# Optimization experiments

Hardware: AMD Instinct MI355X
Metric: run time of the kernel (lower is better)

## Reference

```python
import jax, jax.numpy as jnp
import numpy as np

B, Q, DIM, HEADS, RPE_H, HGRID, WGRID, STRIDE = 2, 900, 256, 8, 512, 64, 64, 16
KV = HGRID * WGRID


def setup_inputs() -> dict:
    key = jax.random.key(0)
    ks = jax.random.split(key, 16)
    s = 0.02
    return {
        "hidden_states": jax.random.normal(ks[0], (B, Q, DIM), jnp.float32),
        "reference_points": jax.random.uniform(ks[1], (B, Q, 1, 4), jnp.float32),
        "key_value_states": jax.random.normal(ks[2], (B, KV, DIM), jnp.float32),
        "spatial_shapes": jnp.array([[HGRID, WGRID]], dtype=jnp.int64),
        "attention_mask": jax.random.randint(ks[3], (B, KV), 0, 2, jnp.int32),
        "mlp1_w1": jax.random.normal(ks[4], (RPE_H, 2), jnp.float32) * s,
        "mlp1_b1": jnp.zeros((RPE_H,), jnp.float32),
        "mlp1_w2": jax.random.normal(ks[5], (HEADS, RPE_H), jnp.float32) * s,
        "mlp2_w1": jax.random.normal(ks[6], (RPE_H, 2), jnp.float32) * s,
        "mlp2_b1": jnp.zeros((RPE_H,), jnp.float32),
        "mlp2_w2": jax.random.normal(ks[7], (HEADS, RPE_H), jnp.float32) * s,
        "q_w": jax.random.normal(ks[8], (DIM, DIM), jnp.float32) * s,
        "q_b": jnp.zeros((DIM,), jnp.float32),
        "k_w": jax.random.normal(ks[9], (DIM, DIM), jnp.float32) * s,
        "k_b": jnp.zeros((DIM,), jnp.float32),
        "v_w": jax.random.normal(ks[10], (DIM, DIM), jnp.float32) * s,
        "v_b": jnp.zeros((DIM,), jnp.float32),
        "o_w": jax.random.normal(ks[11], (DIM, DIM), jnp.float32) * s,
        "o_b": jnp.zeros((DIM,), jnp.float32),
    }


def _attn(hidden_states, reference_points, key_value_states, h, w, attention_mask,
          mlp1_w1, mlp1_b1, mlp1_w2, mlp2_w1, mlp2_b1, mlp2_w2,
          q_w, q_b, k_w, k_b, v_w, v_b, o_w, o_b):
    b, q_len, dim = hidden_states.shape
    nh = mlp1_w2.shape[0]
    hd = dim // nh
    scale = hd ** -0.5
    stride = STRIDE

    # boxes cxcywh -> x1y1x2y2, scaled to absolute pixel coords (reparam=False)
    c, sz = reference_points[..., :2], reference_points[..., 2:]
    ref = jnp.concatenate([c - sz / 2, c + sz / 2], axis=-1)  # (B,Q,1,4)
    mult = jnp.array([w * stride, h * stride, w * stride, h * stride], dtype=ref.dtype)
    ref = ref * mult

    pos_x = (jnp.arange(w, dtype=jnp.float32) + 0.5) * stride
    pos_y = (jnp.arange(h, dtype=jnp.float32) + 0.5) * stride
    dx = ref[..., 0::2] - pos_x[None, None, :, None]  # (B,Q,W,2)
    dy = ref[..., 1::2] - pos_y[None, None, :, None]  # (B,Q,H,2)

    # small MLPs: 2 -> rpe_hidden -> num_heads
    rpe_x = jax.nn.relu(dx @ mlp1_w1.T + mlp1_b1) @ mlp1_w2.T  # (B,Q,W,nh)
    rpe_y = jax.nn.relu(dy @ mlp2_w1.T + mlp2_b1) @ mlp2_w2.T  # (B,Q,H,nh)
    rpe = rpe_x[:, :, None, :, :] + rpe_y[:, :, :, None, :]    # (B,Q,H,W,nh)
    rpe = rpe.reshape(b, q_len, h * w, nh).transpose(0, 3, 1, 2)  # (B,nh,Q,K)

    queries = (hidden_states @ q_w.T + q_b).reshape(b, q_len, nh, hd).transpose(0, 2, 1, 3) * scale
    kv_len = key_value_states.shape[1]
    keys = (key_value_states @ k_w.T + k_b).reshape(b, kv_len, nh, hd).transpose(0, 2, 1, 3)
    values = (key_value_states @ v_w.T + v_b).reshape(b, kv_len, nh, hd).transpose(0, 2, 1, 3)

    scores = jnp.einsum('bhqd,bhkd->bhqk', queries, keys) + rpe
    scores = scores + attention_mask.astype(scores.dtype)[:, None, None] * (-100.0)
    probs = jax.nn.softmax(scores, axis=-1)
    ctx = jnp.einsum('bhqk,bhkd->bhqd', probs, values)
    ctx = ctx.transpose(0, 2, 1, 3).reshape(b, q_len, dim)
    return ctx @ o_w.T + o_b


def reference(hidden_states, reference_points, key_value_states, spatial_shapes, attention_mask,
              mlp1_w1, mlp1_b1, mlp1_w2, mlp2_w1, mlp2_b1, mlp2_w2,
              q_w, q_b, k_w, k_b, v_w, v_b, o_w, o_b):
    h = int(spatial_shapes[0, 0])
    w = int(spatial_shapes[0, 1])
    return _attn(hidden_states, reference_points, key_value_states, h, w, attention_mask,
                 mlp1_w1, mlp1_b1, mlp1_w2, mlp2_w1, mlp2_b1, mlp2_w2,
                 q_w, q_b, k_w, k_b, v_w, v_b, o_w, o_b)
```

## Files before the change

### kernel.cpp

```cpp
#include <hip/hip_runtime.h>
#include <math.h>

#define NB    2
#define NQ    900
#define NQP   960
#define NKV   4096
#define DIMM  256
#define NHEAD 8
#define HD    32
#define RPEH  512
#define GRID  64

#define LOG2E 1.4426950408889634f

typedef short short8 __attribute__((ext_vector_type(8)));
typedef float f32x4 __attribute__((ext_vector_type(4)));
typedef unsigned uint2v __attribute__((ext_vector_type(2)));
typedef unsigned short u16;
typedef unsigned short u16x4 __attribute__((ext_vector_type(4)));

__device__ inline u16 f2bf(float f) {
    unsigned u = __builtin_bit_cast(unsigned, f);
    u += 0x7fff + ((u >> 16) & 1);
    return (u16)(u >> 16);
}
__device__ inline unsigned packbf2(float a, float b) {
    unsigned ua = __builtin_bit_cast(unsigned, a);
    ua += 0x7fff + ((ua >> 16) & 1);
    unsigned ub = __builtin_bit_cast(unsigned, b);
    ub += 0x7fff + ((ub >> 16) & 1);
    return (ua >> 16) | (ub & 0xffff0000u);
}

#define HS4  115200
#define KV4  524288
#define W4   16384
__global__ __launch_bounds__(256) void conv_bf16(
    const float* __restrict__ hs, const float* __restrict__ kv,
    const float* __restrict__ qw, const float* __restrict__ kw,
    const float* __restrict__ vw,
    u16* __restrict__ hsbf, u16* __restrict__ kvbf,
    u16* __restrict__ qwbf, u16* __restrict__ kwbf, u16* __restrict__ vwbf)
{
    const int total = HS4 + KV4 + 3 * W4;
    for (int g = blockIdx.x * 256 + threadIdx.x; g < total; g += gridDim.x * 256) {
        const float* s; u16* d; int off;
        if (g < HS4)                       { s = hs; d = hsbf; off = g; }
        else if (g < HS4 + KV4)            { s = kv; d = kvbf; off = g - HS4; }
        else if (g < HS4 + KV4 + W4)       { s = qw; d = qwbf; off = g - HS4 - KV4; }
        else if (g < HS4 + KV4 + 2 * W4)   { s = kw; d = kwbf; off = g - HS4 - KV4 - W4; }
        else                               { s = vw; d = vwbf; off = g - HS4 - KV4 - 2 * W4; }
        f32x4 v = *(const f32x4*)(s + (size_t)off * 4);
        *(u16x4*)(d + (size_t)off * 4) =
            (u16x4){f2bf(v[0]), f2bf(v[1]), f2bf(v[2]), f2bf(v[3])};
    }
}

__global__ __launch_bounds__(256) void proj_mfma(
    const u16* __restrict__ A,
    const u16* __restrict__ W0, const float* __restrict__ B0,
    const u16* __restrict__ W1, const float* __restrict__ B1,
    u16* __restrict__ outRow, u16* __restrict__ outVt,
    int M, float scale)
{
    __shared__ u16 Abuf[2][4096];
    __shared__ u16 Bbuf[2][4096];

    const u16* W = W0; const float* bias = B0; bool vt = false;
    if (blockIdx.z == 1) { W = W1; bias = B1; vt = true; }

    const int t    = threadIdx.x;
    const int lane = t & 63;
    const int w    = t >> 6;
    const int wm   = w >> 1, wn = w & 1;
    const int m0   = blockIdx.x * 128;
    const int n0   = blockIdx.y * 128;

    const int r0 = t >> 2, c0 = t & 3;
    const int r1 = r0 + 64;
    const int s0 = r0 * 4 + (c0 ^ (r0 & 3));
    const int s1 = r1 * 4 + (c0 ^ (r1 & 3));
    const u16* Arow0 = A + (size_t)(m0 + r0) * DIMM + c0 * 8;
    const u16* Arow1 = A + (size_t)(m0 + r1) * DIMM + c0 * 8;
    const u16* Wrow0 = W + (size_t)(n0 + r0) * DIMM + c0 * 8;
    const u16* Wrow1 = W + (size_t)(n0 + r1) * DIMM + c0 * 8;

    const int fr = lane & 15, fkc = lane >> 4;
    int aslot[4], bslot[4];
    #pragma unroll
    for (int f = 0; f < 4; ++f) {
        int ar = wm * 64 + f * 16 + fr;
        int br = wn * 64 + f * 16 + fr;
        aslot[f] = ar * 4 + (fkc ^ (ar & 3));
        bslot[f] = br * 4 + (fkc ^ (br & 3));
    }
    float bv[4];
    #pragma unroll
    for (int f = 0; f < 4; ++f) bv[f] = bias[n0 + wn * 64 + f * 16 + fr];

    f32x4 acc[4][4] = {};

    {
        short8 a0 = *(const short8*)(Arow0);
        short8 a1 = *(const short8*)(Arow1);
        short8 b0 = *(const short8*)(Wrow0);
        short8 b1 = *(const short8*)(Wrow1);
        *(short8*)&Abuf[0][s0 * 8] = a0;
        *(short8*)&Abuf[0][s1 * 8] = a1;
        *(short8*)&Bbuf[0][s0 * 8] = b0;
        *(short8*)&Bbuf[0][s1 * 8] = b1;
    }
    __syncthreads();

    int cur = 0;
    for (int kt = 0; kt < 8; ++kt) {
        short8 na0, na1, nb0, nb1;
        if (kt < 7) {
            int ko = (kt + 1) * 32;
            na0 = *(const short8*)(Arow0 + ko);
            na1 = *(const short8*)(Arow1 + ko);
            nb0 = *(const short8*)(Wrow0 + ko);
            nb1 = *(const short8*)(Wrow1 + ko);
        }
        short8 af[4], bf[4];
        #pragma unroll
        for (int f = 0; f < 4; ++f) {
            af[f] = *(const short8*)&Abuf[cur][aslot[f] * 8];
            bf[f] = *(const short8*)&Bbuf[cur][bslot[f] * 8];
        }
        #pragma unroll
        for (int i = 0; i < 4; ++i)
            #pragma unroll
            for (int j = 0; j < 4; ++j)
                acc[i][j] = __builtin_amdgcn_mfma_f32_16x16x32_bf16(af[i], bf[j], acc[i][j], 0, 0, 0);
        if (kt < 7) {
            *(short8*)&Abuf[cur ^ 1][s0 * 8] = na0;
            *(short8*)&Abuf[cur ^ 1][s1 * 8] = na1;
            *(short8*)&Bbuf[cur ^ 1][s0 * 8] = nb0;
            *(short8*)&Bbuf[cur ^ 1][s1 * 8] = nb1;
        }
        __syncthreads();
        cur ^= 1;
    }

    #pragma unroll
    for (int i = 0; i < 4; ++i) {
        int mbase = m0 + wm * 64 + i * 16 + 4 * fkc;
        #pragma unroll
        for (int j = 0; j < 4; ++j) {
            int n = n0 + wn * 64 + j * 16 + fr;
            #pragma unroll
            for (int r = 0; r < 4; ++r) {
                int gm = mbase + r;
                if (gm < M) {
                    float v = (acc[i][j][r] + bv[j]) * scale;
                    if (!vt) {
                        outRow[(size_t)gm * DIMM + n] = f2bf(v);
                    } else {
                        int bb = gm >> 12, kvi = gm & 4095;
                        int hh = n >> 5, dd = n & 31;
                        outVt[(size_t)((bb * NHEAD + hh) * HD + dd) * NKV + kvi] = f2bf(v);
                    }
                }
            }
        }
    }
}

__global__ __launch_bounds__(256) void rpe_kernel(
    const float* __restrict__ ref_pts,
    const float* __restrict__ w1x, const float* __restrict__ b1x,
    const float* __restrict__ w2x,
    const float* __restrict__ w1y, const float* __restrict__ b1y,
    const float* __restrict__ w2y,
    float* __restrict__ rpex, float* __restrict__ rpey)
{
    __shared__ f32x4 wpk[RPEH];
    __shared__ float w2t[RPEH][NHEAD];
    __shared__ float2 red[3][4][4][64];

    const int t   = threadIdx.x;
    const int m   = blockIdx.x & 1;
    const int bq0 = (blockIdx.x >> 1) * 4;

    const float* w1 = m ? w1y : w1x;
    const float* b1 = m ? b1y : b1x;
    const float* w2 = m ? w2y : w2x;
    for (int r = t; r < RPEH; r += 256) {
        float a = w1[r * 2], b = w1[r * 2 + 1];
        wpk[r] = (f32x4){a, b, b1[r], a + b};
    }
    for (int i = t; i < RPEH * NHEAD; i += 256) {
        int h = i >> 9, r = i & 511;
        w2t[r][h] = w2[h * RPEH + r] * LOG2E;
    }
    __syncthreads();

    const int lane = t & 63;
    const int wv   = t >> 6;
    const float p  = (lane + 0.5f) * 16.f;

    float lo[4], hi[4];
    #pragma unroll
    for (int j = 0; j < 4; ++j) {
        const float* q = ref_pts + (size_t)(bq0 + j) * 4;
        float c = m ? q[1] : q[0];
        float s = m ? q[3] : q[2];
        lo[j] = (c - s * 0.5f) * 1024.f;
        hi[j] = (c + s * 0.5f) * 1024.f;
    }

    float2 acc[4][4] = {};
    const int r0 = wv * 128;
    #pragma unroll 4
    for (int rr = 0; rr < 128; ++rr) {
        int r = r0 + rr;
        f32x4 W  = wpk[r];
        f32x4 u0 = *(const f32x4*)&w2t[r][0];
        f32x4 u1 = *(const f32x4*)&w2t[r][4];
        float bp = W[3] * p;
        #pragma unroll
        for (int tk = 0; tk < 4; ++tk) {
            float al  = W[0] * lo[tk] + W[1] * hi[tk] + W[2];
            float hid = fmaxf(al - bp, 0.f);
            acc[tk][0].x += u0[0] * hid;  acc[tk][0].y += u0[1] * hid;
            acc[tk][1].x += u0[2] * hid;  acc[tk][1].y += u0[3] * hid;
            acc[tk][2].x += u1[0] * hid;  acc[tk][2].y += u1[1] * hid;
            acc[tk][3].x += u1[2] * hid;  acc[tk][3].y += u1[3] * hid;
        }
    }

    if (wv > 0) {
        #pragma unroll
        for (int tk = 0; tk < 4; ++tk)
            #pragma unroll
            for (int j = 0; j < 4; ++j)
                red[wv - 1][tk][j][lane] = acc[tk][j];
    }
    __syncthreads();
    if (wv == 0) {
        float* outp = m ? rpey : rpex;
        #pragma unroll
        for (int tk = 0; tk < 4; ++tk) {
            size_t base = (size_t)(bq0 + tk) * (NHEAD * GRID) + lane;
            #pragma unroll
            for (int j = 0; j < 4; ++j) {
                float2 s0 = red[0][tk][j][lane];
                float2 s1 = red[1][tk][j][lane];
                float2 s2 = red[2][tk][j][lane];
                float sx = acc[tk][j].x + s0.x + s1.x + s2.x;
                float sy = acc[tk][j].y + s0.y + s1.y + s2.y;
                outp[base + (2 * j) * GRID]     = sx;
                outp[base + (2 * j + 1) * GRID] = sy;
            }
        }
    }
}

template <int SPL>
__global__ __launch_bounds__(256) void attn_mfma(
    const u16* __restrict__ Qbf, const u16* __restrict__ Kbf,
    const u16* __restrict__ Vt,
    const float* __restrict__ RX, const float* __restrict__ RY,
    const int* __restrict__ mask,
    float* __restrict__ pctx, float2* __restrict__ pml)
{
    constexpr int KSEG = NKV / SPL;
    constexpr int NTS  = KSEG / 64;
    __shared__ short8 kbuf[2][4][64];
    __shared__ short8 vbuf[2][4][64];
    __shared__ unsigned pbuf[4][64][4];
    __shared__ float ry_s[NTS][68];
    __shared__ float mbuf[2][64];

    const int tid  = threadIdx.x;
    const int lane = tid & 63;
    const int w    = tid >> 6;
    const int q15  = lane & 15;
    const int g    = lane >> 4;
    const int qt = blockIdx.x, h = blockIdx.y;
    const int b  = blockIdx.z / SPL;
    const int sp = blockIdx.z % SPL;
    const int q0 = qt * 64;
    const int wq = w * 16 + q15;
    const int gq = q0 + wq;
    const bool qok = gq < NQ;
    const int kv0g = sp * KSEG;

    float rxr[16];
    {
        const float* rxrow = RX + (size_t)(b * NQ + (qok ? gq : 0)) * (NHEAD * GRID) + h * GRID;
        #pragma unroll
        for (int kt = 0; kt < 4; ++kt)
            #pragma unroll
            for (int r = 0; r < 4; ++r)
                rxr[kt * 4 + r] = qok ? rxrow[16 * kt + 4 * g + r] : 0.f;
    }
    for (int idx = tid; idx < NTS * 64; idx += 256) {
        int y = idx % NTS, q = idx / NTS;
        int gq2 = q0 + q;
        ry_s[y][q] = (gq2 < NQ)
            ? RY[(size_t)(b * NQ + gq2) * (NHEAD * GRID) + h * GRID + sp * NTS + y] : 0.f;
    }

    short8 qf = *(const short8*)(Qbf + ((size_t)(b * NQ + gq)) * DIMM + h * HD + 8 * g);

    const int sr = tid >> 2, sc = tid & 3;
    const int vd = tid >> 3, vc = tid & 7;
    const size_t kbase = ((size_t)(b * NKV + kv0g + sr)) * DIMM + h * HD + 8 * sc;
    const size_t vbase = ((size_t)((b * NHEAD + h) * HD + vd)) * NKV + kv0g + 8 * vc;

    kbuf[0][sr >> 4][(sr & 15) + 16 * sc] = *(const short8*)(Kbf + kbase);
    vbuf[0][(vc >> 2) * 2 + (vd >> 4)][16 * (vc & 3) + (vd & 15)] = *(const short8*)(Vt + vbase);
    if (tid < 64) mbuf[0][tid] = -(100.f * LOG2E) * (float)mask[b * NKV + kv0g + tid];
    __syncthreads();

    f32x4 cacc0 = {0.f, 0.f, 0.f, 0.f};
    f32x4 cacc1 = {0.f, 0.f, 0.f, 0.f};
    float m_run = -1e30f, l_run = 0.f;
    int cur = 0;

    for (int t = 0; t < NTS; ++t) {
        short8 rk = {}, rv = {};
        float rm = 0.f;
        if (t < NTS - 1) {
            size_t kvn = (size_t)(t + 1) * 64;
            rk = *(const short8*)(Kbf + kbase + kvn * DIMM);
            rv = *(const short8*)(Vt + vbase + kvn);
            if (tid < 64) rm = -(100.f * LOG2E) * (float)mask[b * NKV + kv0g + kvn + tid];
        }

        f32x4 zero = {0.f, 0.f, 0.f, 0.f};
        f32x4 s[4];
        __builtin_amdgcn_s_setprio(1);
        #pragma unroll
        for (int kt = 0; kt < 4; ++kt)
            s[kt] = __builtin_amdgcn_mfma_f32_16x16x32_bf16(kbuf[cur][kt][lane], qf, zero, 0, 0, 0);
        __builtin_amdgcn_s_setprio(0);

        float ryb = ry_s[t][wq];
        #pragma unroll
        for (int kt = 0; kt < 4; ++kt) {
            #pragma unroll
            for (int r = 0; r < 4; ++r)
                s[kt][r] += rxr[kt * 4 + r] + ryb + mbuf[cur][16 * kt + 4 * g + r];
        }

        float mk[4];
        #pragma unroll
        for (int kt = 0; kt < 4; ++kt)
            mk[kt] = fmaxf(fmaxf(s[kt][0], s[kt][1]), fmaxf(s[kt][2], s[kt][3]));
        float mloc = fmaxf(fmaxf(mk[0], mk[1]), fmaxf(mk[2], mk[3]));
        mloc = fmaxf(mloc, __shfl_xor(mloc, 16));
        mloc = fmaxf(mloc, __shfl_xor(mloc, 32));
        float mnew = fmaxf(m_run, mloc);
        float fsc  = exp2f(m_run - mnew);
        float psum = 0.f;
        #pragma unroll
        for (int kt = 0; kt < 4; ++kt)
            #pragma unroll
            for (int r = 0; r < 4; ++r) {
                float pv = exp2f(s[kt][r] - mnew);
                s[kt][r] = pv;
                psum += pv;
            }
        psum += __shfl_xor(psum, 16);
        psum += __shfl_xor(psum, 32);
        l_run = l_run * fsc + psum;
        m_run = mnew;
        cacc0 *= fsc;
        cacc1 *= fsc;

        __builtin_amdgcn_s_setprio(1);
        #pragma unroll
        for (int sk = 0; sk < 2; ++sk) {
            #pragma unroll
            for (int kk = 0; kk < 2; ++kk) {
                int kt = sk * 2 + kk;
                unsigned d0 = packbf2(s[kt][0], s[kt][1]);
                unsigned d1 = packbf2(s[kt][2], s[kt][3]);
                int lt = 16 * ((2 * kt + (g >> 1)) & 3) + q15;
                uint2v* dst = (uint2v*)&pbuf[w][lt][2 * (g & 1)];
                *dst = (uint2v){d0, d1};
            }
            short8 pf = *(const short8*)&pbuf[w][lane][0];
            cacc0 = __builtin_amdgcn_mfma_f32_16x16x32_bf16(vbuf[cur][sk * 2 + 0][lane], pf, cacc0, 0, 0, 0);
            cacc1 = __builtin_amdgcn_mfma_f32_16x16x32_bf16(vbuf[cur][sk * 2 + 1][lane], pf, cacc1, 0, 0, 0);
        }
        __builtin_amdgcn_s_setprio(0);

        if (t < NTS - 1) {
            kbuf[cur ^ 1][sr >> 4][(sr & 15) + 16 * sc] = rk;
            vbuf[cur ^ 1][(vc >> 2) * 2 + (vd >> 4)][16 * (vc & 3) + (vd & 15)] = rv;
            if (tid < 64) mbuf[cur ^ 1][tid] = rm;
        }
        __syncthreads();
        cur ^= 1;
    }

    size_t prow = (size_t)(sp * NB + b) * NQP + gq;
    float* pc = pctx + prow * DIMM + h * HD;
    #pragma unroll
    for (int r = 0; r < 4; ++r) {
        pc[4 * g + r]      = cacc0[r];
        pc[16 + 4 * g + r] = cacc1[r];
    }
    if (g == 0) {
        float2 v; v.x = m_run; v.y = l_run;
        pml[prow * NHEAD + h] = v;
    }
}

template <int SPL>
__global__ __launch_bounds__(256) void attn_reduce(
    const float* __restrict__ pctx, const float2* __restrict__ pml,
    float* __restrict__ CTX)
{
    const int bq = blockIdx.x;
    const int b = bq / NQ, q = bq - b * NQ;
    const int c = threadIdx.x;
    const int h = c >> 5;

    float m[SPL], l[SPL];
    #pragma unroll
    for (int sp = 0; sp < SPL; ++sp) {
        float2 v = pml[((size_t)(sp * NB + b) * NQP + q) * NHEAD + h];
        m[sp] = v.x; l[sp] = v.y;
    }
    float ms = m[0];
    #pragma unroll
    for (int sp = 1; sp < SPL; ++sp) ms = fmaxf(ms, m[sp]);
    float L = 0.f, acc = 0.f;
    #pragma unroll
    for (int sp = 0; sp < SPL; ++sp) {
        float wgt = exp2f(m[sp] - ms);
        L   += wgt * l[sp];
        acc += wgt * pctx[((size_t)(sp * NB + b) * NQP + q) * DIMM + c];
    }
    CTX[(size_t)bq * DIMM + c] = acc / L;
}

__global__ __launch_bounds__(256) void gemm_bias_f32(
    const float* __restrict__ A, const float* __restrict__ W,
    const float* __restrict__ bias, float* __restrict__ C,
    int M, int N, int K)
{
    __shared__ float As[32][33];
    __shared__ float Ws[32][33];
    const int t  = threadIdx.x;
    const int tr = t >> 4;
    const int tc = t & 15;
    const int brow = blockIdx.y * 32;
    const int bcol = blockIdx.x * 32;
    float acc00 = 0.f, acc01 = 0.f, acc10 = 0.f, acc11 = 0.f;

    for (int kt = 0; kt < K; kt += 32) {
        #pragma unroll
        for (int i = 0; i < 4; ++i) {
            int idx = t + i * 256;
            int r = idx >> 5, c = idx & 31;
            int gr = brow + r;
            As[r][c] = (gr < M) ? A[(size_t)gr * K + kt + c] : 0.f;
            Ws[r][c] = W[(size_t)(bcol + r) * K + kt + c];
        }
        __syncthreads();
        #pragma unroll 8
        for (int k = 0; k < 32; ++k) {
            float a0 = As[tr * 2][k], a1 = As[tr * 2 + 1][k];
            float w0 = Ws[tc * 2][k], w1 = Ws[tc * 2 + 1][k];
            acc00 += a0 * w0; acc01 += a0 * w1;
            acc10 += a1 * w0; acc11 += a1 * w1;
        }
        __syncthreads();
    }
    int gc0 = bcol + tc * 2, gc1 = gc0 + 1;
    int gr0 = brow + tr * 2, gr1 = gr0 + 1;
    if (gr0 < M) {
        C[(size_t)gr0 * N + gc0] = acc00 + bias[gc0];
        C[(size_t)gr0 * N + gc1] = acc01 + bias[gc1];
    }
    if (gr1 < M) {
        C[(size_t)gr1 * N + gc0] = acc10 + bias[gc0];
        C[(size_t)gr1 * N + gc1] = acc11 + bias[gc1];
    }
}

extern "C" void kernel_launch(void* const* d_in, const int* in_sizes, int n_in,
                              void* d_out, int out_size, void* d_ws, size_t ws_size,
                              hipStream_t stream)
{
    const float* hs   = (const float*)d_in[0];
    const float* rp   = (const float*)d_in[1];
    const float* kv   = (const float*)d_in[2];
    const int*   msk  = (const int*)d_in[4];
    const float* m1w1 = (const float*)d_in[5];
    const float* m1b1 = (const float*)d_in[6];
    const float* m1w2 = (const float*)d_in[7];
    const float* m2w1 = (const float*)d_in[8];
    const float* m2b1 = (const float*)d_in[9];
    const float* m2w2 = (const float*)d_in[10];
    const float* q_w  = (const float*)d_in[11];
    const float* q_b  = (const float*)d_in[12];
    const float* k_w  = (const float*)d_in[13];
    const float* k_b  = (const float*)d_in[14];
    const float* v_w  = (const float*)d_in[15];
    const float* v_b  = (const float*)d_in[16];
    const float* o_w  = (const float*)d_in[17];
    const float* o_b  = (const float*)d_in[18];
    float* out = (float*)d_out;

    char* p = (char*)d_ws;
    float* RX   = (float*)p; p += (size_t)NB * NQ * NHEAD * GRID * 4;
    float* RY   = (float*)p; p += (size_t)NB * NQ * NHEAD * GRID * 4;
    float* CTX  = (float*)p; p += (size_t)NB * NQ * DIMM * 4;
    u16*   Qbf  = (u16*)p;   p += (size_t)1920 * DIMM * 2;
    u16*   Kbf  = (u16*)p;   p += (size_t)NB * NKV * DIMM * 2;
    u16*   Vt   = (u16*)p;   p += (size_t)NB * NHEAD * HD * NKV * 2;

    char* u = p;
    u16* hsbf = (u16*)u;
    u16* kvbf = hsbf + (size_t)1920 * DIMM;
    u16* qwbf = kvbf + (size_t)NB * NKV * DIMM;
    u16* kwbf = qwbf + (size_t)DIMM * DIMM;
    u16* vwbf = kwbf + (size_t)DIMM * DIMM;
    float* pctx = (float*)u;

    const size_t fixed_bytes = (size_t)(u - (char*)d_ws);
    const size_t need8 = fixed_bytes
                       + (size_t)8 * NB * NQP * DIMM * 4
                       + (size_t)8 * NB * NQP * NHEAD * sizeof(float2);
    const bool use8 = (ws_size >= need8);

    const float scale = 0.17677669529663687f * LOG2E;

    conv_bf16<<<1024, 256, 0, stream>>>(hs, kv, q_w, k_w, v_w,
                                        hsbf, kvbf, qwbf, kwbf, vwbf);

    proj_mfma<<<dim3(15, 2, 1), 256, 0, stream>>>(
        hsbf, qwbf, q_b, nullptr, nullptr, Qbf, nullptr, NB * NQ, scale);

    proj_mfma<<<dim3(64, 2, 2), 256, 0, stream>>>(
        kvbf, kwbf, k_b, vwbf, v_b, Kbf, Vt, NB * NKV, 1.f);

    rpe_kernel<<<900, 256, 0, stream>>>(rp, m1w1, m1b1, m1w2,
                                        m2w1, m2b1, m2w2, RX, RY);

    if (use8) {
        float2* pml = (float2*)(pctx + (size_t)8 * NB * NQP * DIMM);
        attn_mfma<8><<<dim3((NQ + 63) / 64, NHEAD, NB * 8), 256, 0, stream>>>(
            Qbf, Kbf, Vt, RX, RY, msk, pctx, pml);
        attn_reduce<8><<<NB * NQ, 256, 0, stream>>>(pctx, pml, CTX);
    } else {
        float2* pml = (float2*)(pctx + (size_t)4 * NB * NQP * DIMM);
        attn_mfma<4><<<dim3((NQ + 63) / 64, NHEAD, NB * 4), 256, 0, stream>>>(
            Qbf, Kbf, Vt, RX, RY, msk, pctx, pml);
        attn_reduce<4><<<NB * NQ, 256, 0, stream>>>(pctx, pml, CTX);
    }

    gemm_bias_f32<<<dim3(DIMM / 32, (NB * NQ + 31) / 32), 256, 0, stream>>>(
        CTX, o_w, o_b, out, NB * NQ, DIMM, DIMM);
}
```

Before: 149.0 us.

## Add lazy softmax rescaling, hardware bf16 pack, and fix KV split to four

The attention inner loop now rescales the running max, sum and accumulators only when some lane's tile max exceeds the running max by more than a threshold, skipping the exp and multiplies in the common case. The software round-to-nearest bf16 packing is replaced with the v_cvt_pk_bf16_f32 instruction. The split-K path is fixed to four KV segments, dropping the workspace-dependent eight-way path, so fewer blocks run but each does more work. Delaying the rescale lets exponents reach up to 2^8, which could slightly affect bf16 precision of the probabilities.

```diff
diff --git a/kernel.cpp b/kernel.cpp
--- a/kernel.cpp
+++ b/kernel.cpp
@@ -10,6 +10,7 @@
 #define HD    32
 #define RPEH  512
 #define GRID  64
+#define SPLIT 4
 
 #define LOG2E 1.4426950408889634f
 
@@ -24,12 +25,10 @@
     u += 0x7fff + ((u >> 16) & 1);
     return (u16)(u >> 16);
 }
-__device__ inline unsigned packbf2(float a, float b) {
-    unsigned ua = __builtin_bit_cast(unsigned, a);
-    ua += 0x7fff + ((ua >> 16) & 1);
-    unsigned ub = __builtin_bit_cast(unsigned, b);
-    ub += 0x7fff + ((ub >> 16) & 1);
-    return (ua >> 16) | (ub & 0xffff0000u);
+__device__ inline unsigned cvtpk_bf16(float a, float b) {
+    unsigned r;
+    asm("v_cvt_pk_bf16_f32 %0, %1, %2" : "=v"(r) : "v"(a), "v"(b));
+    return r;
 }
 
 #define HS4  115200
@@ -257,7 +256,6 @@
     }
 }
 
-template <int SPL>
 __global__ __launch_bounds__(256) void attn_mfma(
     const u16* __restrict__ Qbf, const u16* __restrict__ Kbf,
     const u16* __restrict__ Vt,
@@ -265,7 +263,7 @@
     const int* __restrict__ mask,
     float* __restrict__ pctx, float2* __restrict__ pml)
 {
-    constexpr int KSEG = NKV / SPL;
+    constexpr int KSEG = NKV / SPLIT;
     constexpr int NTS  = KSEG / 64;
     __shared__ short8 kbuf[2][4][64];
     __shared__ short8 vbuf[2][4][64];
@@ -279,8 +277,8 @@
     const int q15  = lane & 15;
     const int g    = lane >> 4;
     const int qt = blockIdx.x, h = blockIdx.y;
-    const int b  = blockIdx.z / SPL;
-    const int sp = blockIdx.z % SPL;
+    const int b  = blockIdx.z / SPLIT;
+    const int sp = blockIdx.z % SPLIT;
     const int q0 = qt * 64;
     const int wq = w * 16 + q15;
     const int gq = q0 + wq;
@@ -297,7 +295,7 @@
                 rxr[kt * 4 + r] = qok ? rxrow[16 * kt + 4 * g + r] : 0.f;
     }
     for (int idx = tid; idx < NTS * 64; idx += 256) {
-        int y = idx % NTS, q = idx / NTS;
+        int y = idx & (NTS - 1), q = idx / NTS;
         int gq2 = q0 + q;
         ry_s[y][q] = (gq2 < NQ)
             ? RY[(size_t)(b * NQ + gq2) * (NHEAD * GRID) + h * GRID + sp * NTS + y] : 0.f;
@@ -353,23 +351,28 @@
         float mloc = fmaxf(fmaxf(mk[0], mk[1]), fmaxf(mk[2], mk[3]));
         mloc = fmaxf(mloc, __shfl_xor(mloc, 16));
         mloc = fmaxf(mloc, __shfl_xor(mloc, 32));
-        float mnew = fmaxf(m_run, mloc);
-        float fsc  = exp2f(m_run - mnew);
+
+        if (!__all(mloc <= m_run + 8.f)) {
+            float mnew = fmaxf(m_run, mloc);
+            float fsc  = exp2f(m_run - mnew);
+            l_run *= fsc;
+            cacc0 *= fsc;
+            cacc1 *= fsc;
+            m_run = mnew;
+        }
+
         float psum = 0.f;
         #pragma unroll
         for (int kt = 0; kt < 4; ++kt)
             #pragma unroll
             for (int r = 0; r < 4; ++r) {
-                float pv = exp2f(s[kt][r] - mnew);
+                float pv = exp2f(s[kt][r] - m_run);
                 s[kt][r] = pv;
                 psum += pv;
             }
         psum += __shfl_xor(psum, 16);
         psum += __shfl_xor(psum, 32);
-        l_run = l_run * fsc + psum;
-        m_run = mnew;
-        cacc0 *= fsc;
-        cacc1 *= fsc;
+        l_run += psum;
 
         __builtin_amdgcn_s_setprio(1);
         #pragma unroll
@@ -377,8 +380,8 @@
             #pragma unroll
             for (int kk = 0; kk < 2; ++kk) {
                 int kt = sk * 2 + kk;
-                unsigned d0 = packbf2(s[kt][0], s[kt][1]);
-                unsigned d1 = packbf2(s[kt][2], s[kt][3]);
+                unsigned d0 = cvtpk_bf16(s[kt][0], s[kt][1]);
+                unsigned d1 = cvtpk_bf16(s[kt][2], s[kt][3]);
                 int lt = 16 * ((2 * kt + (g >> 1)) & 3) + q15;
                 uint2v* dst = (uint2v*)&pbuf[w][lt][2 * (g & 1)];
                 *dst = (uint2v){d0, d1};
@@ -411,7 +414,6 @@
     }
 }
 
-template <int SPL>
 __global__ __launch_bounds__(256) void attn_reduce(
     const float* __restrict__ pctx, const float2* __restrict__ pml,
     float* __restrict__ CTX)
@@ -421,18 +423,16 @@
     const int c = threadIdx.x;
     const int h = c >> 5;
 
-    float m[SPL], l[SPL];
-    #pragma unroll
-    for (int sp = 0; sp < SPL; ++sp) {
+    float m[SPLIT], l[SPLIT];
+    #pragma unroll
+    for (int sp = 0; sp < SPLIT; ++sp) {
         float2 v = pml[((size_t)(sp * NB + b) * NQP + q) * NHEAD + h];
         m[sp] = v.x; l[sp] = v.y;
     }
-    float ms = m[0];
-    #pragma unroll
-    for (int sp = 1; sp < SPL; ++sp) ms = fmaxf(ms, m[sp]);
+    float ms = fmaxf(fmaxf(m[0], m[1]), fmaxf(m[2], m[3]));
     float L = 0.f, acc = 0.f;
     #pragma unroll
-    for (int sp = 0; sp < SPL; ++sp) {
+    for (int sp = 0; sp < SPLIT; ++sp) {
         float wgt = exp2f(m[sp] - ms);
         L   += wgt * l[sp];
         acc += wgt * pctx[((size_t)(sp * NB + b) * NQP + q) * DIMM + c];
@@ -523,13 +523,8 @@
     u16* qwbf = kvbf + (size_t)NB * NKV * DIMM;
     u16* kwbf = qwbf + (size_t)DIMM * DIMM;
     u16* vwbf = kwbf + (size_t)DIMM * DIMM;
-    float* pctx = (float*)u;
-
-    const size_t fixed_bytes = (size_t)(u - (char*)d_ws);
-    const size_t need8 = fixed_bytes
-                       + (size_t)8 * NB * NQP * DIMM * 4
-                       + (size_t)8 * NB * NQP * NHEAD * sizeof(float2);
-    const bool use8 = (ws_size >= need8);
+    float*  pctx = (float*)u;
+    float2* pml  = (float2*)(pctx + (size_t)SPLIT * NB * NQP * DIMM);
 
     const float scale = 0.17677669529663687f * LOG2E;
 
@@ -545,17 +540,10 @@
     rpe_kernel<<<900, 256, 0, stream>>>(rp, m1w1, m1b1, m1w2,
                                         m2w1, m2b1, m2w2, RX, RY);
 
-    if (use8) {
-        float2* pml = (float2*)(pctx + (size_t)8 * NB * NQP * DIMM);
-        attn_mfma<8><<<dim3((NQ + 63) / 64, NHEAD, NB * 8), 256, 0, stream>>>(
-            Qbf, Kbf, Vt, RX, RY, msk, pctx, pml);
-        attn_reduce<8><<<NB * NQ, 256, 0, stream>>>(pctx, pml, CTX);
-    } else {
-        float2* pml = (float2*)(pctx + (size_t)4 * NB * NQP * DIMM);
-        attn_mfma<4><<<dim3((NQ + 63) / 64, NHEAD, NB * 4), 256, 0, stream>>>(
-            Qbf, Kbf, Vt, RX, RY, msk, pctx, pml);
-        attn_reduce<4><<<NB * NQ, 256, 0, stream>>>(pctx, pml, CTX);
-    }
+    attn_mfma<<<dim3((NQ + 63) / 64, NHEAD, NB * SPLIT), 256, 0, stream>>>(
+        Qbf, Kbf, Vt, RX, RY, msk, pctx, pml);
+
+    attn_reduce<<<NB * NQ, 256, 0, stream>>>(pctx, pml, CTX);
 
     gemm_bias_f32<<<dim3(DIMM / 32, (NB * NQ + 31) / 32), 256, 0, stream>>>(
         CTX, o_w, o_b, out, NB * NQ, DIMM, DIMM);
```

Result: faster. 141.6 us (-5.0%).
